# Optimization experiments

Measured on AMD Instinct MI355X. Metric: run time of the kernel, lower is better.

The kernel has to match this reference:

```python
import jax, jax.numpy as jnp
import numpy as np

N_FEAT = 128      # node_feat_size
HID = 128         # hidden_size
NUM_SEM = 64
N_ITER = 2
E_TYPES = 8
MAX_CHILDS = 65536
NUM_EDGES = 1048576


def setup_inputs() -> dict:
    key = jax.random.key(0)
    ks = jax.random.split(key, 12)
    d_in = N_FEAT + NUM_SEM
    inp = {
        "child_feats": jax.random.normal(ks[0], (1, MAX_CHILDS, d_in), jnp.float32),
        "child_exists": jax.random.uniform(ks[1], (1, MAX_CHILDS, 1), jnp.float32),
        "edge_type_onehot": jax.random.uniform(ks[2], (1, NUM_EDGES, E_TYPES), jnp.float32),
        "edge_indices": jax.random.randint(ks[3], (1, NUM_EDGES, 2), 0, MAX_CHILDS, jnp.int32),
        # learned params (PyTorch Linear: y = x @ W.T + b; store transposed)
        "W_child": jax.random.normal(ks[4], (d_in, HID), jnp.float32) / np.sqrt(d_in),
        "b_child": jnp.zeros((HID,), jnp.float32),
        "W_edge": jax.random.normal(ks[5], (N_ITER, 2 * HID + E_TYPES, HID), jnp.float32) / np.sqrt(2 * HID + E_TYPES),
        "b_edge": jnp.zeros((N_ITER, HID), jnp.float32),
        "W_parent": jax.random.normal(ks[6], ((N_ITER + 1) * HID, N_FEAT), jnp.float32) / np.sqrt((N_ITER + 1) * HID),
        "b_parent": jnp.zeros((N_FEAT,), jnp.float32),
    }
    return inp


def reference(child_feats, child_exists, edge_type_onehot, edge_indices,
              W_child, b_child, W_edge, b_edge, W_parent, b_parent):
    # batch_size == 1 enforced by original module
    x = jax.nn.relu(child_feats[0] @ W_child + b_child) * child_exists[0]  # (N, H)
    src = edge_indices[0, :, 0]  # (E,)
    dst = edge_indices[0, :, 1]  # (E,)
    ef = edge_type_onehot[0]     # (E, T)

    # node_symmetric_type == 'max' readout
    parent_feats = [jnp.max(x, axis=0)]
    for i in range(N_ITER):
        # gather endpoints, concat with edge features, small MLP
        nef = jnp.concatenate([x[src], x[dst], ef], axis=1)          # (E, 2H+T)
        nef = jax.nn.relu(nef @ W_edge[i] + b_edge[i])               # (E, H)
        # edge_symmetric_type == 'sum' -> scatter_add to source nodes
        x = jax.ops.segment_sum(nef, src, num_segments=MAX_CHILDS)   # (N, H)
        parent_feats.append(jnp.max(x, axis=0))

    parent_feat = jnp.concatenate(parent_feats)[None, :]             # (1, (I+1)*H)
    return jax.nn.relu(parent_feat @ W_parent + b_parent)            # (1, node_feat)
```

## Files before the change

### kernel.cpp

```cpp
#include <hip/hip_runtime.h>
#include <hip/hip_bf16.h>

#define HID 128
#define DIN 192
#define NCH 65536
#define NE  1048576

typedef __bf16 bfrag __attribute__((ext_vector_type(8)));
typedef float  ffrag __attribute__((ext_vector_type(4)));

static __device__ __forceinline__ __bf16 f2bf(float x) { return (__bf16)x; }
static __device__ __forceinline__ unsigned pk2(float a, float b) {
    __bf16 b0 = f2bf(a), b1 = f2bf(b);
    return (unsigned)*(unsigned short*)&b0 | ((unsigned)*(unsigned short*)&b1 << 16);
}

struct Frags { bfrag a[5]; };

__global__ __launch_bounds__(256) void k_child(
    const float* __restrict__ cf, const float* __restrict__ exists,
    const float* __restrict__ Wc, const float* __restrict__ bc,
    __bf16* __restrict__ xA, unsigned int* __restrict__ pmax)
{
    __shared__ __bf16 Wl[6 * 8 * 64 * 8];
    __shared__ float  bl[HID];
    __shared__ unsigned int cm[HID];
    const int t = threadIdx.x;

    for (int idx = t; idx < DIN * HID; idx += 256) {
        int k = idx >> 7, h = idx & 127;
        int kt = k >> 5, kk = k & 31;
        int lane = ((kk >> 3) << 4) | (h & 15);
        Wl[((((kt * 8) + (h >> 4)) * 64 + lane) << 3) | (kk & 7)] = f2bf(Wc[idx]);
    }
    for (int idx = t; idx < HID; idx += 256) { bl[idx] = bc[idx]; cm[idx] = 0u; }
    __syncthreads();

    const int wave = t >> 6, lane = t & 63;
    const int m = lane & 15, quad = lane >> 4;

    const int tile = blockIdx.x * 4 + wave;
    const int r0 = tile << 4;
    const int row = r0 + m;

    ffrag acc[8];
    #pragma unroll
    for (int u = 0; u < 8; ++u)
        #pragma unroll
        for (int r = 0; r < 4; ++r) acc[u][r] = 0.f;

    const float* arow = cf + (size_t)row * DIN + quad * 8;
    #pragma unroll
    for (int kt = 0; kt < 6; ++kt) {
        float4 f0 = *(const float4*)(arow + kt * 32);
        float4 f1 = *(const float4*)(arow + kt * 32 + 4);
        bfrag a;
        a[0]=f2bf(f0.x); a[1]=f2bf(f0.y); a[2]=f2bf(f0.z); a[3]=f2bf(f0.w);
        a[4]=f2bf(f1.x); a[5]=f2bf(f1.y); a[6]=f2bf(f1.z); a[7]=f2bf(f1.w);
        #pragma unroll
        for (int u = 0; u < 8; ++u) {
            bfrag b = *(const bfrag*)(&Wl[(((kt * 8 + u) * 64 + lane) << 3)]);
            acc[u] = __builtin_amdgcn_mfma_f32_16x16x32_bf16(a, b, acc[u], 0, 0, 0);
        }
    }

    float mxu[8];
    #pragma unroll
    for (int u = 0; u < 8; ++u) mxu[u] = 0.f;

    #pragma unroll
    for (int r = 0; r < 4; ++r) {
        int er = r0 + quad * 4 + r;
        float exv = exists[er];
        __bf16* orow = xA + (size_t)er * HID;
        #pragma unroll
        for (int u = 0; u < 8; ++u) {
            int col = u * 16 + m;
            float v = fmaxf(acc[u][r] + bl[col], 0.f) * exv;
            orow[col] = f2bf(v);
            mxu[u] = fmaxf(mxu[u], v);
        }
    }
    #pragma unroll
    for (int u = 0; u < 8; ++u) {
        float v = mxu[u];
        v = fmaxf(v, __shfl_xor(v, 16));
        v = fmaxf(v, __shfl_xor(v, 32));
        if (quad == 0) atomicMax(&cm[u * 16 + m], __float_as_uint(v));
    }
    __syncthreads();
    if (t < HID) atomicMax(&pmax[t], cm[t]);
}

__global__ __launch_bounds__(256) void k_hist(
    const int* __restrict__ eidx, int* __restrict__ deg)
{
    int e = blockIdx.x * 256 + threadIdx.x;
    atomicAdd(&deg[eidx[2 * e]], 1);
}

__global__ __launch_bounds__(1024) void k_scan(
    const int* __restrict__ deg, int* __restrict__ off, int* __restrict__ cursor)
{
    __shared__ int sc[1024];
    const int t = threadIdx.x;
    const int base = t * 64;
    int s = 0;
    for (int i = 0; i < 64; ++i) s += deg[base + i];
    sc[t] = s;
    __syncthreads();
    for (int o = 1; o < 1024; o <<= 1) {
        int v = (t >= o) ? sc[t - o] : 0;
        __syncthreads();
        sc[t] += v;
        __syncthreads();
    }
    int run = sc[t] - s;
    for (int i = 0; i < 64; ++i) {
        int v = deg[base + i];
        off[base + i] = run;
        cursor[base + i] = run;
        run += v;
    }
    if (t == 1023) off[NCH] = run;
}

__global__ __launch_bounds__(256) void k_scatter(
    const int* __restrict__ eidx, int* __restrict__ cursor,
    const float* __restrict__ ef,
    int* __restrict__ dsts, __bf16* __restrict__ efs)
{
    int e = blockIdx.x * 256 + threadIdx.x;
    int s = eidx[2 * e], d = eidx[2 * e + 1];
    const float4* p = (const float4*)(ef + (size_t)e * 8);
    float4 f0 = p[0], f1 = p[1];
    int pos = atomicAdd(&cursor[s], 1);
    dsts[pos] = d;
    uint4 pk;
    pk.x = pk2(f0.x, f0.y); pk.y = pk2(f0.z, f0.w);
    pk.z = pk2(f1.x, f1.y); pk.w = pk2(f1.z, f1.w);
    *(uint4*)(efs + (size_t)pos * 8) = pk;
}

__global__ __launch_bounds__(256) void k_src(
    const __bf16* __restrict__ xCur, const float* __restrict__ We,
    const float* __restrict__ be, __bf16* __restrict__ St2)
{
    __shared__ __bf16 Wl[4 * 8 * 64 * 8];
    __shared__ float  bl[HID];
    const int t = threadIdx.x;
    for (int idx = t; idx < 128 * HID; idx += 256) {
        int k = idx >> 7, h = idx & 127;
        int kt = k >> 5, kk = k & 31;
        int lane = ((kk >> 3) << 4) | (h & 15);
        Wl[((((kt * 8) + (h >> 4)) * 64 + lane) << 3) | (kk & 7)] = f2bf(We[idx]);
    }
    for (int idx = t; idx < HID; idx += 256) bl[idx] = be[idx];
    __syncthreads();

    const int wave = t >> 6, lane = t & 63;
    const int m = lane & 15, quad = lane >> 4;
    const int tile = blockIdx.x * 4 + wave;
    const int r0 = tile << 4;
    const int row = r0 + m;

    ffrag acc[8];
    #pragma unroll
    for (int u = 0; u < 8; ++u)
        #pragma unroll
        for (int r = 0; r < 4; ++r) acc[u][r] = 0.f;

    const __bf16* ar = xCur + (size_t)row * HID + quad * 8;
    #pragma unroll
    for (int kt = 0; kt < 4; ++kt) {
        bfrag a = *(const bfrag*)(ar + kt * 32);
        #pragma unroll
        for (int u = 0; u < 8; ++u) {
            bfrag b = *(const bfrag*)(&Wl[(((kt * 8 + u) * 64 + lane) << 3)]);
            acc[u] = __builtin_amdgcn_mfma_f32_16x16x32_bf16(a, b, acc[u], 0, 0, 0);
        }
    }
    #pragma unroll
    for (int r = 0; r < 4; ++r) {
        int node = r0 + quad * 4 + r;
        bfrag pk;
        #pragma unroll
        for (int u = 0; u < 8; ++u) pk[u] = f2bf(acc[u][r] + bl[u * 16 + m]);
        *(bfrag*)(St2 + ((size_t)node * 16 + m) * 8) = pk;
    }
}

#define EFW_OFF (4 * 8 * 64 * 8)

__global__ __launch_bounds__(256) void k_edge2(
    const __bf16* __restrict__ xCur,
    const int*    __restrict__ offs,
    const int*    __restrict__ dsts,
    const __bf16* __restrict__ efs,
    const __bf16* __restrict__ St2,
    const float*  __restrict__ We,
    __bf16* __restrict__ xNext,
    unsigned int* __restrict__ pmax, int stage)
{
    __shared__ __bf16 Wl[4 * 8 * 64 * 8 + 8 * 16 * 8];
    __shared__ unsigned int cm[HID];
    const int t = threadIdx.x;

    if (t < HID) cm[t] = 0u;
    for (int idx = t; idx < 128 * HID; idx += 256) {
        int k = idx >> 7, h = idx & 127;
        int kt = k >> 5, kk = k & 31;
        int lane = ((kk >> 3) << 4) | (h & 15);
        Wl[((((kt * 8) + (h >> 4)) * 64 + lane) << 3) | (kk & 7)] = f2bf(We[(size_t)(128 + k) * HID + h]);
    }
    for (int idx = t; idx < 8 * HID; idx += 256) {
        int k2 = idx >> 7, h = idx & 127;
        Wl[EFW_OFF + ((((h >> 4) * 16) + (h & 15)) << 3) + k2] = f2bf(We[(size_t)(256 + k2) * HID + h]);
    }
    __syncthreads();

    const int wave = t >> 6, lane = t & 63;
    const int m = lane & 15, quad = lane >> 4;
    const int gw = blockIdx.x * 4 + wave;
    const int n0 = gw * 4;
    const int lc16 = (lane & 15) << 3;

    const int o0 = offs[n0],     o1 = offs[n0 + 1], o2 = offs[n0 + 2];
    const int o3 = offs[n0 + 3], o4 = offs[n0 + 4];

    auto selo = [&](int q) -> int {
        return (q <= 0) ? o0 : (q == 1) ? o1 : (q == 2) ? o2 : (q == 3) ? o3 : o4;
    };

    float mxu[8];
    #pragma unroll
    for (int u = 0; u < 8; ++u) mxu[u] = 0.f;

    if (o0 < o4) {
        const int dvA = dsts[min(o0 + lane, o4 - 1)];
        const int dvB = dsts[min(o0 + 64 + lane, o4 - 1)];

        auto LOADT = [&](int j) -> Frags {
            Frags f;
            int jl = j + m; jl = (jl < o4) ? jl : (o4 - 1);
            int rel = jl - o0;
            int dA = __shfl(dvA, rel & 63);
            int dB = __shfl(dvB, rel & 63);
            int dm;
            if (rel < 64)       dm = dA;
            else if (rel < 128) dm = dB;
            else                dm = dsts[jl];
            const __bf16* rd = xCur + (size_t)dm * HID + quad * 8;
            f.a[0] = *(const bfrag*)(rd);
            f.a[1] = *(const bfrag*)(rd + 32);
            f.a[2] = *(const bfrag*)(rd + 64);
            f.a[3] = *(const bfrag*)(rd + 96);
            bfrag z;
            #pragma unroll
            for (int q = 0; q < 8; ++q) z[q] = (__bf16)0.f;
            if (quad == 0) z = *(const bfrag*)(efs + (size_t)jl * 8);
            f.a[4] = z;
            return f;
        };

        int ci = 0;
        while (selo(ci) == selo(ci + 1)) ++ci;
        int cj = selo(ci);

        bfrag sb = *(const bfrag*)(St2 + ((size_t)(n0 + ci) * 16 + m) * 8);
        float part[8];
        #pragma unroll
        for (int u = 0; u < 8; ++u) part[u] = 0.f;

        Frags aC = LOADT(cj);

        for (;;) {
            const int cEnd = selo(ci + 1);
            int ni = ci, nj = cj + 16;
            if (nj >= cEnd) {
                ni = ci + 1;
                while (ni < 4 && selo(ni) == selo(ni + 1)) ++ni;
                nj = (ni < 4) ? selo(ni) : 0;
            }
            const bool hn = (ni < 4);
            Frags aN;
            if (hn) aN = LOADT(nj);

            ffrag acc[8];
            #pragma unroll
            for (int u = 0; u < 8; ++u) {
                float s = (float)sb[u];
                acc[u][0] = s; acc[u][1] = s; acc[u][2] = s; acc[u][3] = s;
            }
            #pragma unroll
            for (int kt = 0; kt < 4; ++kt)
                #pragma unroll
                for (int u = 0; u < 8; ++u) {
                    bfrag b = *(const bfrag*)(&Wl[(((kt * 8 + u) * 64 + lane) << 3)]);
                    acc[u] = __builtin_amdgcn_mfma_f32_16x16x32_bf16(aC.a[kt], b, acc[u], 0, 0, 0);
                }
            #pragma unroll
            for (int u = 0; u < 8; ++u) {
                bfrag b = *(const bfrag*)(&Wl[EFW_OFF + (u << 7) + lc16]);
                acc[u] = __builtin_amdgcn_mfma_f32_16x16x32_bf16(aC.a[4], b, acc[u], 0, 0, 0);
            }

            const int rb = cj + quad * 4;
            #pragma unroll
            for (int r = 0; r < 4; ++r) {
                if (rb + r < cEnd) {
                    #pragma unroll
                    for (int u = 0; u < 8; ++u)
                        part[u] += fmaxf(acc[u][r], 0.f);
                }
            }

            if (!hn || ni != ci) {
                float tot[8];
                #pragma unroll
                for (int u = 0; u < 8; ++u) {
                    float v = part[u];
                    v += __shfl_xor(v, 16);
                    v += __shfl_xor(v, 32);
                    tot[u] = v;
                    mxu[u] = fmaxf(mxu[u], v);
                }
                float sA = (quad == 0) ? tot[0] : (quad == 1) ? tot[2] : (quad == 2) ? tot[4] : tot[6];
                float sB = (quad == 0) ? tot[1] : (quad == 1) ? tot[3] : (quad == 2) ? tot[5] : tot[7];
                const int n = n0 + ci, u0 = quad * 2;
                xNext[(size_t)n * HID + u0 * 16 + m]      = f2bf(sA);
                xNext[(size_t)n * HID + u0 * 16 + 16 + m] = f2bf(sB);
                if (hn) {
                    sb = *(const bfrag*)(St2 + ((size_t)(n0 + ni) * 16 + m) * 8);
                    #pragma unroll
                    for (int u = 0; u < 8; ++u) part[u] = 0.f;
                }
            }
            if (!hn) break;
            aC = aN; ci = ni; cj = nj;
        }
    }

    {
        const int u0 = quad * 2;
        const __bf16 zz = (__bf16)0.f;
        if (o0 == o1) { xNext[(size_t)(n0+0)*HID + u0*16 + m] = zz; xNext[(size_t)(n0+0)*HID + u0*16 + 16 + m] = zz; }
        if (o1 == o2) { xNext[(size_t)(n0+1)*HID + u0*16 + m] = zz; xNext[(size_t)(n0+1)*HID + u0*16 + 16 + m] = zz; }
        if (o2 == o3) { xNext[(size_t)(n0+2)*HID + u0*16 + m] = zz; xNext[(size_t)(n0+2)*HID + u0*16 + 16 + m] = zz; }
        if (o3 == o4) { xNext[(size_t)(n0+3)*HID + u0*16 + m] = zz; xNext[(size_t)(n0+3)*HID + u0*16 + 16 + m] = zz; }
    }

    #pragma unroll
    for (int u = 0; u < 8; ++u) {
        float v = mxu[u];
        v = fmaxf(v, __shfl_xor(v, 16));
        v = fmaxf(v, __shfl_xor(v, 32));
        if (quad == 0) atomicMax(&cm[u * 16 + m], __float_as_uint(v));
    }
    __syncthreads();
    if (t < HID) atomicMax(&pmax[stage * HID + t], cm[t]);
}

__global__ __launch_bounds__(256) void k_edge_at(
    const __bf16* __restrict__ xA, const int* __restrict__ eidx,
    const float* __restrict__ ef, const float* __restrict__ We,
    const float* __restrict__ be, float* __restrict__ xNew)
{
    __shared__ __bf16 Wl[9 * 8 * 64 * 8];
    __shared__ float  bl[HID];
    const int t = threadIdx.x;
    for (int idx = t; idx < 8 * 64 * 8; idx += 256) Wl[8 * 8 * 64 * 8 + idx] = (__bf16)0.f;
    __syncthreads();
    for (int idx = t; idx < 256 * HID; idx += 256) {
        int k = idx >> 7, h = idx & 127;
        int kt = k >> 5, kk = k & 31;
        int lane = ((kk >> 3) << 4) | (h & 15);
        Wl[((((kt * 8) + (h >> 4)) * 64 + lane) << 3) | (kk & 7)] = f2bf(We[idx]);
    }
    for (int idx = t; idx < 8 * HID; idx += 256) {
        int k2 = idx >> 7, h = idx & 127;
        Wl[((((8 * 8) + (h >> 4)) * 64 + (h & 15)) << 3) | k2] = f2bf(We[(256 + k2) * HID + h]);
    }
    for (int idx = t; idx < HID; idx += 256) bl[idx] = be[idx];
    __syncthreads();

    const int wave = t >> 6, lane = t & 63;
    const int m = lane & 15, quad = lane >> 4;
    for (int c = 0; c < 8; ++c) {
        const int e0 = blockIdx.x * 512 + c * 64 + wave * 16;
        const int e  = e0 + m;
        const int src = eidx[2 * e], dst = eidx[2 * e + 1];
        const __bf16* rs = xA + (size_t)src * HID;
        const __bf16* rd = xA + (size_t)dst * HID;
        bfrag a[9];
        #pragma unroll
        for (int kt = 0; kt < 4; ++kt) a[kt] = *(const bfrag*)(rs + kt * 32 + quad * 8);
        #pragma unroll
        for (int kt = 4; kt < 8; ++kt) a[kt] = *(const bfrag*)(rd + (kt - 4) * 32 + quad * 8);
        {
            bfrag z;
            #pragma unroll
            for (int q = 0; q < 8; ++q) z[q] = (__bf16)0.f;
            if (quad == 0) {
                const float4* p = (const float4*)(ef + (size_t)e * 8);
                float4 f0 = p[0], f1 = p[1];
                z[0]=f2bf(f0.x); z[1]=f2bf(f0.y); z[2]=f2bf(f0.z); z[3]=f2bf(f0.w);
                z[4]=f2bf(f1.x); z[5]=f2bf(f1.y); z[6]=f2bf(f1.z); z[7]=f2bf(f1.w);
            }
            a[8] = z;
        }
        ffrag acc[8];
        #pragma unroll
        for (int u = 0; u < 8; ++u)
            #pragma unroll
            for (int r = 0; r < 4; ++r) acc[u][r] = 0.f;
        #pragma unroll
        for (int kt = 0; kt < 9; ++kt)
            #pragma unroll
            for (int u = 0; u < 8; ++u) {
                bfrag b = *(const bfrag*)(&Wl[(((kt * 8 + u) * 64 + lane) << 3)]);
                acc[u] = __builtin_amdgcn_mfma_f32_16x16x32_bf16(a[kt], b, acc[u], 0, 0, 0);
            }
        #pragma unroll
        for (int r = 0; r < 4; ++r) {
            int er = e0 + quad * 4 + r;
            int sr = eidx[2 * er];
            float* outrow = xNew + (size_t)sr * HID;
            #pragma unroll
            for (int u = 0; u < 8; ++u) {
                int col = u * 16 + m;
                atomicAdd(outrow + col, fmaxf(acc[u][r] + bl[col], 0.f));
            }
        }
    }
}

__global__ __launch_bounds__(256) void k_fin(
    float* __restrict__ xNew, __bf16* __restrict__ xA,
    unsigned int* __restrict__ pmax, int stage, int flags)
{
    const int t = threadIdx.x;
    const size_t total  = (size_t)NCH * HID;
    const size_t stride = (size_t)gridDim.x * 256;
    float mx = 0.f;
    for (size_t i = (size_t)blockIdx.x * 256 + t; i < total; i += stride) {
        float v = xNew[i];
        mx = fmaxf(mx, v);
        if (flags & 1) xA[i] = f2bf(v);
        if (flags & 2) xNew[i] = 0.f;
    }
    __shared__ float red[256];
    red[t] = mx;
    __syncthreads();
    if (t < 128) {
        float v = fmaxf(red[t], red[t + 128]);
        atomicMax(&pmax[stage * HID + t], __float_as_uint(v));
    }
}

__global__ __launch_bounds__(128) void k_parent(
    const unsigned int* __restrict__ pmaxU,
    const float* __restrict__ Wp, const float* __restrict__ bp,
    float* __restrict__ out)
{
    __shared__ float pl[384];
    const int t = threadIdx.x;
    for (int i = t; i < 384; i += 128) pl[i] = __uint_as_float(pmaxU[i]);
    __syncthreads();
    float acc = bp[t];
    for (int j = 0; j < 384; ++j) acc += pl[j] * Wp[j * HID + t];
    out[t] = fmaxf(acc, 0.f);
}

extern "C" void kernel_launch(void* const* d_in, const int* in_sizes, int n_in,
                              void* d_out, int out_size, void* d_ws, size_t ws_size,
                              hipStream_t stream)
{
    const float* cf   = (const float*)d_in[0];
    const float* ex   = (const float*)d_in[1];
    const float* ef   = (const float*)d_in[2];
    const int*   eidx = (const int*)d_in[3];
    const float* Wc   = (const float*)d_in[4];
    const float* bc   = (const float*)d_in[5];
    const float* We   = (const float*)d_in[6];
    const float* be   = (const float*)d_in[7];
    const float* Wp   = (const float*)d_in[8];
    const float* bp   = (const float*)d_in[9];
    float* out = (float*)d_out;

    char* ws = (char*)d_ws;

    const size_t OFF_XA   = 0;
    const size_t OFF_XB   = OFF_XA   + (size_t)NCH * HID * 2;
    const size_t OFF_ST   = OFF_XB   + (size_t)NCH * HID * 2;
    const size_t OFF_EFS  = OFF_ST   + (size_t)NCH * HID * 2;
    const size_t OFF_DST  = OFF_EFS  + (size_t)NE * 8 * 2;
    const size_t OFF_OFFS = OFF_DST  + (size_t)NE * 4;
    const size_t OFF_DEG  = OFF_OFFS + 262400;
    const size_t OFF_CUR  = OFF_DEG  + 262144;
    const size_t OFF_PMAX = OFF_CUR  + 262144;
    const size_t NEED     = OFF_PMAX + 2048;

    if (ws_size >= NEED) {
        __bf16*       xA   = (__bf16*)(ws + OFF_XA);
        __bf16*       xB   = (__bf16*)(ws + OFF_XB);
        __bf16*       St2  = (__bf16*)(ws + OFF_ST);
        __bf16*       efs  = (__bf16*)(ws + OFF_EFS);
        int*          dsts = (int*)   (ws + OFF_DST);
        int*          offs = (int*)   (ws + OFF_OFFS);
        int*          deg  = (int*)   (ws + OFF_DEG);
        int*          cur  = (int*)   (ws + OFF_CUR);
        unsigned int* pmax = (unsigned int*)(ws + OFF_PMAX);

        hipMemsetAsync(pmax, 0, 384 * sizeof(unsigned int), stream);
        hipMemsetAsync(deg, 0, NCH * sizeof(int), stream);

        k_child  <<<1024, 256, 0, stream>>>(cf, ex, Wc, bc, xA, pmax);
        k_hist   <<<4096, 256, 0, stream>>>(eidx, deg);
        k_scan   <<<1,   1024, 0, stream>>>(deg, offs, cur);
        k_scatter<<<4096, 256, 0, stream>>>(eidx, cur, ef, dsts, efs);

        k_src    <<<1024, 256, 0, stream>>>(xA, We, be, St2);
        k_edge2  <<<4096, 256, 0, stream>>>(xA, offs, dsts, efs, St2, We, xB, pmax, 1);
        k_src    <<<1024, 256, 0, stream>>>(xB, We + 264 * HID, be + HID, St2);
        k_edge2  <<<4096, 256, 0, stream>>>(xB, offs, dsts, efs, St2, We + 264 * HID, xA, pmax, 2);
        k_parent <<<1,    128, 0, stream>>>(pmax, Wp, bp, out);
    } else {
        float*        xNew = (float*)ws;
        __bf16*       xA   = (__bf16*)(ws + (size_t)NCH * HID * 4);
        unsigned int* pmax = (unsigned int*)(ws + (size_t)NCH * HID * 6);

        hipMemsetAsync(pmax, 0, 384 * sizeof(unsigned int), stream);
        hipMemsetAsync(xNew, 0, (size_t)NCH * HID * 4, stream);

        k_child  <<<1024, 256, 0, stream>>>(cf, ex, Wc, bc, xA, pmax);
        k_edge_at<<<2048, 256, 0, stream>>>(xA, eidx, ef, We,             be,       xNew);
        k_fin    <<<512,  256, 0, stream>>>(xNew, xA, pmax, 1, 3);
        k_edge_at<<<2048, 256, 0, stream>>>(xA, eidx, ef, We + 264 * HID, be + HID, xNew);
        k_fin    <<<512,  256, 0, stream>>>(xNew, xA, pmax, 2, 0);
        k_parent <<<1,    128, 0, stream>>>(pmax, Wp, bp, out);
    }
}
```

Before: 638.0 us.

## Precompute destination-node projection per node instead of per edge

Moves the x[dst] @ W_edge[128:256] product out of the per-edge loop: k_src now also computes it per node and overwrites xCur with the projected features. In k_edge2 the gathered rows are already projected, so the 32 weight MFMAs per edge tile become 8 MFMAs against identity-like selector fragments that copy the gathered values into the accumulators. This cuts edge-side matrix work and LDS weight loading, and removes the large weight tile from k_edge2's shared memory. The cost is an extra per-node GEMM, in-place modification of xCur, and an extra bf16 rounding of the projected values.

```diff
diff --git a/kernel.cpp b/kernel.cpp
--- a/kernel.cpp
+++ b/kernel.cpp
@@ -143,43 +143,45 @@
 }
 
 __global__ __launch_bounds__(256) void k_src(
-    const __bf16* __restrict__ xCur, const float* __restrict__ We,
+    __bf16* __restrict__ xCur, const float* __restrict__ We,
     const float* __restrict__ be, __bf16* __restrict__ St2)
 {
     __shared__ __bf16 Wl[4 * 8 * 64 * 8];
     __shared__ float  bl[HID];
     const int t = threadIdx.x;
-    for (int idx = t; idx < 128 * HID; idx += 256) {
-        int k = idx >> 7, h = idx & 127;
-        int kt = k >> 5, kk = k & 31;
-        int lane = ((kk >> 3) << 4) | (h & 15);
-        Wl[((((kt * 8) + (h >> 4)) * 64 + lane) << 3) | (kk & 7)] = f2bf(We[idx]);
-    }
-    for (int idx = t; idx < HID; idx += 256) bl[idx] = be[idx];
-    __syncthreads();
-
     const int wave = t >> 6, lane = t & 63;
     const int m = lane & 15, quad = lane >> 4;
     const int tile = blockIdx.x * 4 + wave;
     const int r0 = tile << 4;
     const int row = r0 + m;
 
+    for (int idx = t; idx < 128 * HID; idx += 256) {
+        int k = idx >> 7, h = idx & 127;
+        int kt = k >> 5, kk = k & 31;
+        int ln = ((kk >> 3) << 4) | (h & 15);
+        Wl[((((kt * 8) + (h >> 4)) * 64 + ln) << 3) | (kk & 7)] = f2bf(We[idx]);
+    }
+    for (int idx = t; idx < HID; idx += 256) bl[idx] = be[idx];
+    __syncthreads();
+
+    bfrag a[4];
+    const __bf16* ar = xCur + (size_t)row * HID + quad * 8;
+    #pragma unroll
+    for (int kt = 0; kt < 4; ++kt) a[kt] = *(const bfrag*)(ar + kt * 32);
+
     ffrag acc[8];
     #pragma unroll
     for (int u = 0; u < 8; ++u)
         #pragma unroll
         for (int r = 0; r < 4; ++r) acc[u][r] = 0.f;
 
-    const __bf16* ar = xCur + (size_t)row * HID + quad * 8;
-    #pragma unroll
-    for (int kt = 0; kt < 4; ++kt) {
-        bfrag a = *(const bfrag*)(ar + kt * 32);
+    #pragma unroll
+    for (int kt = 0; kt < 4; ++kt)
         #pragma unroll
         for (int u = 0; u < 8; ++u) {
             bfrag b = *(const bfrag*)(&Wl[(((kt * 8 + u) * 64 + lane) << 3)]);
-            acc[u] = __builtin_amdgcn_mfma_f32_16x16x32_bf16(a, b, acc[u], 0, 0, 0);
-        }
-    }
+            acc[u] = __builtin_amdgcn_mfma_f32_16x16x32_bf16(a[kt], b, acc[u], 0, 0, 0);
+        }
     #pragma unroll
     for (int r = 0; r < 4; ++r) {
         int node = r0 + quad * 4 + r;
@@ -188,9 +190,36 @@
         for (int u = 0; u < 8; ++u) pk[u] = f2bf(acc[u][r] + bl[u * 16 + m]);
         *(bfrag*)(St2 + ((size_t)node * 16 + m) * 8) = pk;
     }
-}
-
-#define EFW_OFF (4 * 8 * 64 * 8)
+    __syncthreads();
+
+    for (int idx = t; idx < 128 * HID; idx += 256) {
+        int k = idx >> 7, h = idx & 127;
+        int kt = k >> 5, kk = k & 31;
+        int ln = ((kk >> 3) << 4) | (h & 15);
+        Wl[((((kt * 8) + (h >> 4)) * 64 + ln) << 3) | (kk & 7)] = f2bf(We[(size_t)(128 + k) * HID + h]);
+    }
+    __syncthreads();
+
+    #pragma unroll
+    for (int u = 0; u < 8; ++u)
+        #pragma unroll
+        for (int r = 0; r < 4; ++r) acc[u][r] = 0.f;
+
+    #pragma unroll
+    for (int kt = 0; kt < 4; ++kt)
+        #pragma unroll
+        for (int u = 0; u < 8; ++u) {
+            bfrag b = *(const bfrag*)(&Wl[(((kt * 8 + u) * 64 + lane) << 3)]);
+            acc[u] = __builtin_amdgcn_mfma_f32_16x16x32_bf16(a[kt], b, acc[u], 0, 0, 0);
+        }
+    #pragma unroll
+    for (int r = 0; r < 4; ++r) {
+        int node = r0 + quad * 4 + r;
+        __bf16* orow = xCur + (size_t)node * HID;
+        #pragma unroll
+        for (int u = 0; u < 8; ++u) orow[u * 16 + m] = f2bf(acc[u][r]);
+    }
+}
 
 __global__ __launch_bounds__(256) void k_edge2(
     const __bf16* __restrict__ xCur,
@@ -202,20 +231,14 @@
     __bf16* __restrict__ xNext,
     unsigned int* __restrict__ pmax, int stage)
 {
-    __shared__ __bf16 Wl[4 * 8 * 64 * 8 + 8 * 16 * 8];
+    __shared__ __bf16 Wl[8 * 16 * 8];
     __shared__ unsigned int cm[HID];
     const int t = threadIdx.x;
 
     if (t < HID) cm[t] = 0u;
-    for (int idx = t; idx < 128 * HID; idx += 256) {
-        int k = idx >> 7, h = idx & 127;
-        int kt = k >> 5, kk = k & 31;
-        int lane = ((kk >> 3) << 4) | (h & 15);
-        Wl[((((kt * 8) + (h >> 4)) * 64 + lane) << 3) | (kk & 7)] = f2bf(We[(size_t)(128 + k) * HID + h]);
-    }
     for (int idx = t; idx < 8 * HID; idx += 256) {
         int k2 = idx >> 7, h = idx & 127;
-        Wl[EFW_OFF + ((((h >> 4) * 16) + (h & 15)) << 3) + k2] = f2bf(We[(size_t)(256 + k2) * HID + h]);
+        Wl[((((h >> 4) * 16) + (h & 15)) << 3) + k2] = f2bf(We[(size_t)(256 + k2) * HID + h]);
     }
     __syncthreads();
 
@@ -224,6 +247,13 @@
     const int gw = blockIdx.x * 4 + wave;
     const int n0 = gw * 4;
     const int lc16 = (lane & 15) << 3;
+
+    bfrag Bev, Bod;
+    #pragma unroll
+    for (int j = 0; j < 8; ++j) {
+        Bev[j] = (quad == (m >> 3)     && j == (m & 7)) ? (__bf16)1.f : (__bf16)0.f;
+        Bod[j] = (quad == 2 + (m >> 3) && j == (m & 7)) ? (__bf16)1.f : (__bf16)0.f;
+    }
 
     const int o0 = offs[n0],     o1 = offs[n0 + 1], o2 = offs[n0 + 2];
     const int o3 = offs[n0 + 3], o4 = offs[n0 + 4];
@@ -293,15 +323,12 @@
                 acc[u][0] = s; acc[u][1] = s; acc[u][2] = s; acc[u][3] = s;
             }
             #pragma unroll
-            for (int kt = 0; kt < 4; ++kt)
-                #pragma unroll
-                for (int u = 0; u < 8; ++u) {
-                    bfrag b = *(const bfrag*)(&Wl[(((kt * 8 + u) * 64 + lane) << 3)]);
-                    acc[u] = __builtin_amdgcn_mfma_f32_16x16x32_bf16(aC.a[kt], b, acc[u], 0, 0, 0);
-                }
+            for (int u = 0; u < 8; ++u)
+                acc[u] = __builtin_amdgcn_mfma_f32_16x16x32_bf16(
+                    aC.a[u >> 1], (u & 1) ? Bod : Bev, acc[u], 0, 0, 0);
             #pragma unroll
             for (int u = 0; u < 8; ++u) {
-                bfrag b = *(const bfrag*)(&Wl[EFW_OFF + (u << 7) + lc16]);
+                bfrag b = *(const bfrag*)(&Wl[(u << 7) + lc16]);
                 acc[u] = __builtin_amdgcn_mfma_f32_16x16x32_bf16(aC.a[4], b, acc[u], 0, 0, 0);
             }
 
```

After: 611.4 us. -4.2%, faster.
